# Kernel tuning notes

Measured on AMD Instinct MI355X. Metric: run time of the kernel, lower is better.

The kernel has to match this reference:

```python
import jax, jax.numpy as jnp
import numpy as np

B, S, D, H = 8, 1024, 512, 12
HS = D // H  # 42 (head_size; 12*42 = 504 concat width, as in the original)


def setup_inputs() -> dict:
    key = jax.random.key(0)
    ks = jax.random.split(key, 12)
    sd = 0.02
    return {
        "embedded_patches": jax.random.normal(ks[0], (B, S, D), dtype=jnp.float32),
        # stacked per-head projections (12 independent Linear(D, HS, bias=False))
        "wk": jax.random.normal(ks[1], (H, D, HS), dtype=jnp.float32) * sd,
        "wq": jax.random.normal(ks[2], (H, D, HS), dtype=jnp.float32) * sd,
        "wv": jax.random.normal(ks[3], (H, D, HS), dtype=jnp.float32) * sd,
        "w_proj": jax.random.normal(ks[4], (H * HS, D), dtype=jnp.float32) * sd,  # [504, 512]
        "b_proj": jnp.zeros((D,), dtype=jnp.float32),
        # shared LayerNorm (same params used for both norms, as in the original)
        "gamma": jnp.ones((D,), dtype=jnp.float32),
        "beta": jnp.zeros((D,), dtype=jnp.float32),
        "w1": jax.random.normal(ks[5], (D, 4 * D), dtype=jnp.float32) * sd,
        "b1": jnp.zeros((4 * D,), dtype=jnp.float32),
        "w2": jax.random.normal(ks[6], (4 * D, D), dtype=jnp.float32) * sd,
        "b2": jnp.zeros((D,), dtype=jnp.float32),
    }


def _layernorm(x, gamma, beta, eps=1e-5):
    mu = jnp.mean(x, axis=-1, keepdims=True)
    var = jnp.var(x, axis=-1, keepdims=True)
    return (x - mu) * jax.lax.rsqrt(var + eps) * gamma + beta


def reference(embedded_patches, wk, wq, wv, w_proj, b_proj, gamma, beta, w1, b1, w2, b2):
    x = embedded_patches
    n1 = _layernorm(x, gamma, beta)
    # per-head projections, vectorized over heads: [B,S,D] x [H,D,E] -> [B,H,S,E]
    q = jnp.einsum('bsd,hde->bhse', n1, wq)
    k = jnp.einsum('bsd,hde->bhse', n1, wk)
    v = jnp.einsum('bsd,hde->bhse', n1, wv)
    scale = HS ** -0.5
    wei = jax.nn.softmax(jnp.einsum('bhse,bhte->bhst', q, k) * scale, axis=-1)
    out = jnp.einsum('bhst,bhte->bhse', wei, v)        # [B,H,S,E]
    out = out.transpose(0, 2, 1, 3).reshape(B, S, H * HS)  # concat heads -> [B,S,504]
    attn = out @ w_proj + b_proj                       # [B,S,D]
    # original quirk: takes batch element 0 and broadcasts against residual
    first_added = attn[0] + x                          # [S,D] + [B,S,D] -> [B,S,D]
    n2 = _layernorm(first_added, gamma, beta)
    h = jax.nn.gelu(n2 @ w1 + b1, approximate=False)   # torch nn.GELU default = exact erf
    ff = h @ w2 + b2
    return ff + first_added
```

## Files before the change

### kernel.cpp

```cpp
#include <hip/hip_runtime.h>
#include <hip/hip_bf16.h>
#include <stdint.h>


typedef unsigned short u16;
typedef __attribute__((ext_vector_type(8))) short short8;
typedef __attribute__((ext_vector_type(4))) float f32x4;

__device__ __forceinline__ u16 f2bf(float f) {
  union { float f; unsigned u; } x; x.f = f;
  return (u16)((x.u + 0x7FFFu + ((x.u >> 16) & 1u)) >> 16);
}
__device__ __forceinline__ float bf2f(u16 u) {
  union { unsigned u; float f; } x; x.u = ((unsigned)u) << 16;
  return x.f;
}

__device__ __forceinline__ void gload_lds16(const u16* g, u16* l) {
  __builtin_amdgcn_global_load_lds(
      (__attribute__((address_space(1))) void*)g,
      (__attribute__((address_space(3))) void*)l, 16, 0, 0);
}

__device__ __forceinline__ float wred_sum(float v) {
#pragma unroll
  for (int off = 32; off > 0; off >>= 1) v += __shfl_xor(v, off, 64);
  return v;
}

__device__ __forceinline__ float gelu_fast(float t) {
  const float p = __builtin_fmaf(0.0356774081f, t * t, 0.7978845608f);
  return t / (1.0f + __expf(-2.0f * t * p));
}

#define MFMA16x16(a, b, c) __builtin_amdgcn_mfma_f32_16x16x32_bf16(a, b, c, 0, 0, 0)

enum { EP_BF16 = 0, EP_F32B = 2, EP_GELU = 3, EP_ATOM = 7 };

template <int EP, int TM>
__device__ __forceinline__ void gemm_core(u16* lds, const u16* __restrict__ Ab,
                                          int lda, const u16* __restrict__ Bb,
                                          int ldb, void* __restrict__ Cv,
                                          int ldc, int K,
                                          const float* __restrict__ bias,
                                          int m0, int n0) {
  constexpr int ASZ = TM * 32;
  u16* lA[2] = {lds, lds + ASZ};
  u16* lB[2] = {lds + 2 * ASZ, lds + 2 * ASZ + 4096};

  const int tid = threadIdx.x;
  const int w = tid >> 6;
  const int l = tid & 63;
  const int wr = w >> 1;
  const int wc = w & 1;
  const int NT = K >> 5;

  f32x4 acc[4][4];
#pragma unroll
  for (int i = 0; i < 4; ++i)
#pragma unroll
    for (int j = 0; j < 4; ++j) acc[i][j] = (f32x4){0.f, 0.f, 0.f, 0.f};

  const int sk = (l & 3) * 8;
  const u16* gA = Ab + (long)(m0 + w * 32 + (l >> 2)) * lda + sk;
  const int dOffA = w * 1024;
  const int srowB = (TM == 128) ? (w * 32 + (l >> 2)) : (w * 16 + (l >> 2));
  const u16* gB = Bb + (long)(n0 + srowB) * ldb + sk;
  const int dOffB = (TM == 128) ? w * 1024 : w * 512;

  const int aoff = (wr * 64 + (l & 15)) * 32 + (l >> 4) * 8;
  const int boff = (wc * 64 + (l & 15)) * 32 + (l >> 4) * 8;

  auto stage = [&](int b_, int t_) {
    const int k0 = t_ * 32;
    gload_lds16(gA + k0, lA[b_] + dOffA);
    gload_lds16(gA + k0 + 16 * lda, lA[b_] + dOffA + 512);
    gload_lds16(gB + k0, lB[b_] + dOffB);
    if (TM == 128) gload_lds16(gB + k0 + 16 * ldb, lB[b_] + dOffB + 512);
  };

  stage(0, 0);
  __syncthreads();

  int buf = 0;
  for (int t = 0; t < NT; ++t) {
    short8 af[4], bfv[4];
#pragma unroll
    for (int mi = 0; mi < 4; ++mi)
      af[mi] = *(const short8*)&lA[buf][aoff + mi * 16 * 32];
#pragma unroll
    for (int ni = 0; ni < 4; ++ni)
      bfv[ni] = *(const short8*)&lB[buf][boff + ni * 16 * 32];
    if (t + 1 < NT) stage(buf ^ 1, t + 1);
#pragma unroll
    for (int mi = 0; mi < 4; ++mi)
#pragma unroll
      for (int ni = 0; ni < 4; ++ni)
        acc[mi][ni] = MFMA16x16(af[mi], bfv[ni], acc[mi][ni]);
    __syncthreads();
    buf ^= 1;
  }

  const int rbase = m0 + wr * 64 + (l >> 4) * 4;
  const int cbase = n0 + wc * 64 + (l & 15);
#pragma unroll
  for (int mi = 0; mi < 4; ++mi) {
#pragma unroll
    for (int ni = 0; ni < 4; ++ni) {
#pragma unroll
      for (int j = 0; j < 4; ++j) {
        const int row = rbase + mi * 16 + j;
        const int col = cbase + ni * 16;
        const float v = acc[mi][ni][j];
        if (EP == EP_BF16) {
          ((u16*)Cv)[(long)row * ldc + col] = f2bf(v);
        } else if (EP == EP_F32B) {
          ((float*)Cv)[(long)row * ldc + col] = v + bias[col];
        } else if (EP == EP_GELU) {
          ((u16*)Cv)[(long)row * ldc + col] = f2bf(gelu_fast(v + bias[col]));
        } else {
          atomicAdd(&((float*)Cv)[(long)row * ldc + col], v);
        }
      }
    }
  }
}

template <int EP, int TM>
__launch_bounds__(TM * 2, 2)
__global__ void gemm_k(const u16* __restrict__ A, int lda, long sAz,
                       const u16* __restrict__ Bt, int ldb, long sBz,
                       void* __restrict__ Cv, int ldc, int K,
                       const float* __restrict__ bias) {
  __shared__ u16 lds[2 * TM * 32 + 2 * 128 * 32];
  const int gx = gridDim.x, gy = gridDim.y, gz = gridDim.z;
  const int lin = blockIdx.x + gx * (blockIdx.y + gy * blockIdx.z);
  const int nwg = gx * gy * gz;
  const int wg = (lin & 7) * (nwg >> 3) + (lin >> 3);
  const int by = wg % gy;
  const int rem = wg / gy;
  const int z = rem % gz;
  const int bx = rem / gz;
  const u16* Ab = A + (long)z * sAz;
  const u16* Bb = Bt + (long)z * sBz;
  gemm_core<EP, TM>(lds, Ab, lda, Bb, ldb, Cv, ldc, K, bias, bx * TM,
                    by * 128);
}

__launch_bounds__(256, 4)
__global__ void qkvt_kernel(const u16* __restrict__ n1,
                            const u16* __restrict__ BtQKV,
                            u16* __restrict__ qkvc,
                            const u16* __restrict__ wvT,
                            u16* __restrict__ vt) {
  __shared__ u16 lds[4 * 128 * 32];
  const int lin = blockIdx.x;
  const int wg = (lin & 7) * 24 + (lin >> 3);
  if (wg < 96) {
    gemm_core<EP_BF16, 128>(lds, n1, 512, BtQKV, 512, qkvc, 1536, 512,
                            nullptr, (wg & 7) * 128, (wg >> 3) * 128);
  } else {
    const int v = wg - 96;
    gemm_core<EP_BF16, 128>(lds, wvT, 512, n1, 512, vt, 1024, 512, nullptr,
                            (v % 12) * 128, (v / 12) * 128);
  }
}

__device__ __forceinline__ short8 frag_read(const u16* base, int row, int ks,
                                            int l) {
  const int g = (ks * 4 + (l >> 4)) ^ (l & 7);
  return *(const short8*)&base[row * 64 + g * 8];
}

__launch_bounds__(256, 2)
__global__ void flash_attn(const u16* __restrict__ qkvc,
                           const u16* __restrict__ vt,
                           u16* __restrict__ cat) {
  __shared__ u16 lQ[64 * 64];
  __shared__ u16 lK[2][64 * 64];
  __shared__ u16 lV[2][64 * 64];
  __shared__ u16 lP[4][16 * 64];
  const int h = blockIdx.x;
  const int q0 = blockIdx.y * 64;
  const int tid = threadIdx.x;
  const int w = tid >> 6;
  const int l = tid & 63;
  const int sg = ((l & 7) ^ (l >> 3)) * 8;
  const int sr = w * 8 + (l >> 3);

#define FA_STAGE(t_, b_)                                                    \
  do {                                                                      \
    const int kv_ = (t_) * 64;                                              \
    gload_lds16(qkvc + (long)(kv_ + sr) * 1536 + 768 + h * 64 + sg,         \
                lK[b_] + w * 8 * 64);                                       \
    gload_lds16(qkvc + (long)(kv_ + 32 + sr) * 1536 + 768 + h * 64 + sg,    \
                lK[b_] + (32 + w * 8) * 64);                                \
    gload_lds16(vt + (long)(h * 128 + sr) * 1024 + kv_ + sg,                \
                lV[b_] + w * 8 * 64);                                       \
    gload_lds16(vt + (long)(h * 128 + 32 + sr) * 1024 + kv_ + sg,           \
                lV[b_] + (32 + w * 8) * 64);                                \
  } while (0)

  gload_lds16(qkvc + (long)(q0 + sr) * 1536 + h * 64 + sg, lQ + w * 8 * 64);
  gload_lds16(qkvc + (long)(q0 + 32 + sr) * 1536 + h * 64 + sg,
              lQ + (32 + w * 8) * 64);
  FA_STAGE(0, 0);
  __syncthreads();

  const short8 qf0 = frag_read(lQ, w * 16 + (l & 15), 0, l);
  const short8 qf1 = frag_read(lQ, w * 16 + (l & 15), 1, l);

  f32x4 accO[4];
  float m_run[4], l_run[4];
#pragma unroll
  for (int i = 0; i < 4; ++i) {
    accO[i] = (f32x4){0.f, 0.f, 0.f, 0.f};
    m_run[i] = -3.0e38f;
    l_run[i] = 0.f;
  }

  int buf = 0;
  for (int t = 0; t < 16; ++t) {
    if (t + 1 < 16) FA_STAGE(t + 1, buf ^ 1);
    f32x4 s[4];
#pragma unroll
    for (int ni = 0; ni < 4; ++ni) {
      const short8 kf0 = frag_read(lK[buf], ni * 16 + (l & 15), 0, l);
      const short8 kf1 = frag_read(lK[buf], ni * 16 + (l & 15), 1, l);
      s[ni] = MFMA16x16(qf0, kf0, ((f32x4){0.f, 0.f, 0.f, 0.f}));
      s[ni] = MFMA16x16(qf1, kf1, s[ni]);
    }
#pragma unroll
    for (int j = 0; j < 4; ++j) {
      float mx = fmaxf(fmaxf(s[0][j], s[1][j]), fmaxf(s[2][j], s[3][j]));
      mx = fmaxf(mx, __shfl_xor(mx, 1));
      mx = fmaxf(mx, __shfl_xor(mx, 2));
      mx = fmaxf(mx, __shfl_xor(mx, 4));
      mx = fmaxf(mx, __shfl_xor(mx, 8));
      const float mn = fmaxf(m_run[j], mx);
      const float corr = __expf(m_run[j] - mn);
      m_run[j] = mn;
      float ps = 0.f;
#pragma unroll
      for (int ni = 0; ni < 4; ++ni) {
        const float p = __expf(s[ni][j] - mn);
        s[ni][j] = p;
        ps += p;
      }
      ps += __shfl_xor(ps, 1);
      ps += __shfl_xor(ps, 2);
      ps += __shfl_xor(ps, 4);
      ps += __shfl_xor(ps, 8);
      l_run[j] = l_run[j] * corr + ps;
#pragma unroll
      for (int ne = 0; ne < 4; ++ne) accO[ne][j] *= corr;
    }
#pragma unroll
    for (int ni = 0; ni < 4; ++ni) {
#pragma unroll
      for (int j = 0; j < 4; ++j) {
        const int row = (l >> 4) * 4 + j;
        const int col = ni * 16 + (l & 15);
        const int boff = row * 128 + (((col >> 3) ^ (row & 7)) << 4) +
                         (col & 7) * 2;
        *(u16*)((char*)lP[w] + boff) = f2bf(s[ni][j]);
      }
    }
    asm volatile("s_waitcnt lgkmcnt(0)" ::: "memory");
    __builtin_amdgcn_sched_barrier(0);
    const short8 pf0 = frag_read(lP[w], (l & 15), 0, l);
    const short8 pf1 = frag_read(lP[w], (l & 15), 1, l);
#pragma unroll
    for (int ne = 0; ne < 4; ++ne) {
      const short8 vf0 = frag_read(lV[buf], ne * 16 + (l & 15), 0, l);
      const short8 vf1 = frag_read(lV[buf], ne * 16 + (l & 15), 1, l);
      accO[ne] = MFMA16x16(pf0, vf0, accO[ne]);
      accO[ne] = MFMA16x16(pf1, vf1, accO[ne]);
    }
    __syncthreads();
    buf ^= 1;
  }
#undef FA_STAGE

#pragma unroll
  for (int j = 0; j < 4; ++j) {
    const float inv = 1.0f / l_run[j];
    const int row = q0 + w * 16 + (l >> 4) * 4 + j;
#pragma unroll
    for (int ne = 0; ne < 4; ++ne) {
      const int e = ne * 16 + (l & 15);
      if (e < 42)
        cat[(long)row * 512 + h * 42 + e] = f2bf(accO[ne][j] * inv);
    }
  }
}

__device__ __forceinline__ void transpose_body(const float* __restrict__ in,
                                               u16* __restrict__ out, int N,
                                               int Kin, int Kpad, int blk,
                                               int gx, int t, float* smem) {
  const int n0 = (blk % gx) * 64;
  const int k0 = (blk / gx) * 64;
  const int tc = t & 63;
  const int tr = t >> 6;
#pragma unroll
  for (int r = 0; r < 16; ++r) {
    const int kr = tr * 16 + r;
    const int kg = k0 + kr;
    smem[kr * 65 + tc] = (kg < Kin) ? in[(long)kg * N + n0 + tc] : 0.f;
  }
  __syncthreads();
  const int nr0 = t >> 4;
  const int kc = (t & 15) * 4;
#pragma unroll
  for (int p = 0; p < 4; ++p) {
    const int nr = nr0 + p * 16;
    ushort4 v;
    v.x = f2bf(smem[(kc + 0) * 65 + nr]);
    v.y = f2bf(smem[(kc + 1) * 65 + nr]);
    v.z = f2bf(smem[(kc + 2) * 65 + nr]);
    v.w = f2bf(smem[(kc + 3) * 65 + nr]);
    *(ushort4*)&out[(long)(n0 + nr) * Kpad + k0 + kc] = v;
  }
}

__global__ void prep_fused(const float* __restrict__ wq,
                           const float* __restrict__ wk,
                           const float* __restrict__ wv,
                           const float* __restrict__ w_proj,
                           const float* __restrict__ w1,
                           const float* __restrict__ w2,
                           const float* __restrict__ x,
                           const float* __restrict__ gamma,
                           const float* __restrict__ beta,
                           u16* __restrict__ BtQKV, u16* __restrict__ wvT,
                           u16* __restrict__ BtP, u16* __restrict__ Bt1,
                           u16* __restrict__ Bt2, u16* __restrict__ cat,
                           u16* __restrict__ n1, float scale) {
  __shared__ float smem[64 * 65];
  const int blk = blockIdx.x;
  const int t = threadIdx.x;
  if (blk < 3072) {
    const int i = blk * 256 + t;
    const int n = i >> 9, d = i & 511;
    const int pq = n / 768;
    const int h = (n % 768) >> 6;
    const int e = n & 63;
    float v = 0.f;
    if (e < 42) {
      v = (pq ? wk : wq)[((long)h * 512 + d) * 42 + e];
      if (!pq) v *= scale;
    }
    BtQKV[i] = f2bf(v);
  } else if (blk < 6144) {
    const int i = (blk - 3072) * 256 + t;
    const int r = i >> 9, d = i & 511;
    const int h = r >> 7, e = r & 127;
    wvT[i] = f2bf(e < 42 ? wv[((long)h * 512 + d) * 42 + e] : 0.f);
  } else if (blk < 6208) {
    transpose_body(w_proj, BtP, 512, 504, 512, blk - 6144, 8, t, smem);
  } else if (blk < 6464) {
    transpose_body(w1, Bt1, 2048, 512, 512, blk - 6208, 32, t, smem);
  } else if (blk < 6720) {
    transpose_body(w2, Bt2, 512, 2048, 2048, blk - 6464, 8, t, smem);
  } else if (blk < 8768) {
    cat[(blk - 6720) * 256 + t] = 0;
  } else {
    const int s = blk - 8768;
    const float* row = x + (long)s * 512;
    const float v0 = row[t];
    const float v1 = row[t + 256];
    float sum = wred_sum(v0 + v1);
    float sq = wred_sum(v0 * v0 + v1 * v1);
    if ((t & 63) == 0) { smem[t >> 6] = sum; smem[8 + (t >> 6)] = sq; }
    __syncthreads();
    sum = smem[0] + smem[1] + smem[2] + smem[3];
    sq = smem[8] + smem[9] + smem[10] + smem[11];
    const float mu = sum * (1.0f / 512.0f);
    const float rstd = rsqrtf(sq * (1.0f / 512.0f) - mu * mu + 1e-5f);
    n1[(long)s * 512 + t] = f2bf((v0 - mu) * rstd * gamma[t] + beta[t]);
    n1[(long)s * 512 + t + 256] =
        f2bf((v1 - mu) * rstd * gamma[t + 256] + beta[t + 256]);
  }
}

__global__ void ln2_kernel(const float* __restrict__ x,
                           const float* __restrict__ aproj,
                           const float* __restrict__ gamma,
                           const float* __restrict__ beta,
                           const float* __restrict__ b2,
                           u16* __restrict__ n2, float* __restrict__ outp) {
  __shared__ float red[16];
  const int r = blockIdx.x;
  const int t = threadIdx.x;
  const int s = r & 1023;
  const float* xr = x + (long)r * 512;
  const float* ar = aproj + (long)s * 512;
  const float v0 = xr[t] + ar[t];
  const float v1 = xr[t + 256] + ar[t + 256];
  outp[(long)r * 512 + t] = v0 + b2[t];
  outp[(long)r * 512 + t + 256] = v1 + b2[t + 256];
  float sum = wred_sum(v0 + v1);
  float sq = wred_sum(v0 * v0 + v1 * v1);
  if ((t & 63) == 0) { red[t >> 6] = sum; red[8 + (t >> 6)] = sq; }
  __syncthreads();
  sum = red[0] + red[1] + red[2] + red[3];
  sq = red[8] + red[9] + red[10] + red[11];
  const float mu = sum * (1.0f / 512.0f);
  const float rstd = rsqrtf(sq * (1.0f / 512.0f) - mu * mu + 1e-5f);
  n2[(long)r * 512 + t] = f2bf((v0 - mu) * rstd * gamma[t] + beta[t]);
  n2[(long)r * 512 + t + 256] =
      f2bf((v1 - mu) * rstd * gamma[t + 256] + beta[t + 256]);
}

extern "C" void kernel_launch(void* const* d_in, const int* in_sizes, int n_in,
                              void* d_out, int out_size, void* d_ws,
                              size_t ws_size, hipStream_t stream) {
  const float* x = (const float*)d_in[0];
  const float* wk = (const float*)d_in[1];
  const float* wq = (const float*)d_in[2];
  const float* wv = (const float*)d_in[3];
  const float* w_proj = (const float*)d_in[4];
  const float* b_proj = (const float*)d_in[5];
  const float* gamma = (const float*)d_in[6];
  const float* beta = (const float*)d_in[7];
  const float* w1 = (const float*)d_in[8];
  const float* b1 = (const float*)d_in[9];
  const float* w2 = (const float*)d_in[10];
  const float* b2 = (const float*)d_in[11];

  char* base = (char*)d_ws;
  size_t off = 0;
  auto alloc = [&](size_t bytes) -> void* {
    void* p = base + off;
    off += (bytes + 255) & ~(size_t)255;
    return p;
  };
  u16* n1 = (u16*)alloc(1024L * 512 * 2);
  u16* qkvc = (u16*)alloc(1024L * 1536 * 2);
  u16* wvT = (u16*)alloc(1536L * 512 * 2);
  u16* vt = (u16*)alloc(1536L * 1024 * 2);
  u16* cat = (u16*)alloc(1024L * 512 * 2);
  float* aproj = (float*)alloc(1024L * 512 * 4);
  u16* n2 = (u16*)alloc(8192L * 512 * 2);
  u16* hbuf = (u16*)alloc(8192L * 2048 * 2);
  u16* BtQKV = (u16*)alloc(1536L * 512 * 2);
  u16* BtP = (u16*)alloc(512L * 512 * 2);
  u16* Bt1 = (u16*)alloc(2048L * 512 * 2);
  u16* Bt2 = (u16*)alloc(512L * 2048 * 2);
  (void)ws_size; (void)in_sizes; (void)n_in; (void)out_size;

  const float scale = 0.15430334996209191f;

  prep_fused<<<9792, 256, 0, stream>>>(wq, wk, wv, w_proj, w1, w2, x, gamma,
                                       beta, BtQKV, wvT, BtP, Bt1, Bt2, cat,
                                       n1, scale);
  qkvt_kernel<<<192, 256, 0, stream>>>(n1, BtQKV, qkvc, wvT, vt);
  flash_attn<<<dim3(12, 16), 256, 0, stream>>>(qkvc, vt, cat);
  gemm_k<EP_F32B, 128><<<dim3(8, 4, 1), 256, 0, stream>>>(
      cat, 512, 0, BtP, 512, 0, aproj, 512, 512, b_proj);
  ln2_kernel<<<8192, 256, 0, stream>>>(x, aproj, gamma, beta, b2, n2,
                                       (float*)d_out);
  gemm_k<EP_GELU, 256><<<dim3(32, 16, 1), 512, 0, stream>>>(
      n2, 512, 0, Bt1, 512, 0, hbuf, 2048, 512, b1);
  gemm_k<EP_ATOM, 256><<<dim3(32, 4, 2), 512, 0, stream>>>(
      hbuf, 2048, 1024, Bt2, 2048, 1024, d_out, 512, 1024, nullptr);
}
```

Before: 173.0 us.

## Use 128x128 GEMM tiles everywhere and restructure weight-prep transposes through LDS

Drops the 256-row tile variant so the FFN GEMMs run as 256-thread 128x128 workgroups (twice as many blocks), with launch bounds raised to 5 waves per SIMD for more occupancy. The QKV and V weight repacking now stages 64-row slabs in shared memory so both reads and writes are coalesced, using far fewer blocks. The cat buffer zeroing now clears only the 8 padding columns, since attention writes the rest. This trades per-tile reuse of B loads in the FFN GEMMs for better occupancy and load balance, and cuts prep-kernel memory traffic.

New measurement: 377.3 us. +118.1%, slower.

```diff
diff --git a/kernel.cpp b/kernel.cpp
--- a/kernel.cpp
+++ b/kernel.cpp
@@ -37,16 +37,15 @@
 
 enum { EP_BF16 = 0, EP_F32B = 2, EP_GELU = 3, EP_ATOM = 7 };
 
-template <int EP, int TM>
+template <int EP>
 __device__ __forceinline__ void gemm_core(u16* lds, const u16* __restrict__ Ab,
                                           int lda, const u16* __restrict__ Bb,
                                           int ldb, void* __restrict__ Cv,
                                           int ldc, int K,
                                           const float* __restrict__ bias,
                                           int m0, int n0) {
-  constexpr int ASZ = TM * 32;
-  u16* lA[2] = {lds, lds + ASZ};
-  u16* lB[2] = {lds + 2 * ASZ, lds + 2 * ASZ + 4096};
+  u16* lA[2] = {lds, lds + 4096};
+  u16* lB[2] = {lds + 8192, lds + 12288};
 
   const int tid = threadIdx.x;
   const int w = tid >> 6;
@@ -61,22 +60,21 @@
 #pragma unroll
     for (int j = 0; j < 4; ++j) acc[i][j] = (f32x4){0.f, 0.f, 0.f, 0.f};
 
+  const int srow = w * 32 + (l >> 2);
   const int sk = (l & 3) * 8;
-  const u16* gA = Ab + (long)(m0 + w * 32 + (l >> 2)) * lda + sk;
-  const int dOffA = w * 1024;
-  const int srowB = (TM == 128) ? (w * 32 + (l >> 2)) : (w * 16 + (l >> 2));
-  const u16* gB = Bb + (long)(n0 + srowB) * ldb + sk;
-  const int dOffB = (TM == 128) ? w * 1024 : w * 512;
+  const u16* gA = Ab + (long)(m0 + srow) * lda + sk;
+  const u16* gB = Bb + (long)(n0 + srow) * ldb + sk;
+  const int dOff = w * 1024;
 
   const int aoff = (wr * 64 + (l & 15)) * 32 + (l >> 4) * 8;
   const int boff = (wc * 64 + (l & 15)) * 32 + (l >> 4) * 8;
 
   auto stage = [&](int b_, int t_) {
     const int k0 = t_ * 32;
-    gload_lds16(gA + k0, lA[b_] + dOffA);
-    gload_lds16(gA + k0 + 16 * lda, lA[b_] + dOffA + 512);
-    gload_lds16(gB + k0, lB[b_] + dOffB);
-    if (TM == 128) gload_lds16(gB + k0 + 16 * ldb, lB[b_] + dOffB + 512);
+    gload_lds16(gA + k0, lA[b_] + dOff);
+    gload_lds16(gA + k0 + 16 * lda, lA[b_] + dOff + 512);
+    gload_lds16(gB + k0, lB[b_] + dOff);
+    gload_lds16(gB + k0 + 16 * ldb, lB[b_] + dOff + 512);
   };
 
   stage(0, 0);
@@ -126,13 +124,13 @@
   }
 }
 
-template <int EP, int TM>
-__launch_bounds__(TM * 2, 2)
+template <int EP>
+__launch_bounds__(256, 5)
 __global__ void gemm_k(const u16* __restrict__ A, int lda, long sAz,
                        const u16* __restrict__ Bt, int ldb, long sBz,
                        void* __restrict__ Cv, int ldc, int K,
                        const float* __restrict__ bias) {
-  __shared__ u16 lds[2 * TM * 32 + 2 * 128 * 32];
+  __shared__ u16 lds[4 * 128 * 32];
   const int gx = gridDim.x, gy = gridDim.y, gz = gridDim.z;
   const int lin = blockIdx.x + gx * (blockIdx.y + gy * blockIdx.z);
   const int nwg = gx * gy * gz;
@@ -143,11 +141,10 @@
   const int bx = rem / gz;
   const u16* Ab = A + (long)z * sAz;
   const u16* Bb = Bt + (long)z * sBz;
-  gemm_core<EP, TM>(lds, Ab, lda, Bb, ldb, Cv, ldc, K, bias, bx * TM,
-                    by * 128);
-}
-
-__launch_bounds__(256, 4)
+  gemm_core<EP>(lds, Ab, lda, Bb, ldb, Cv, ldc, K, bias, bx * 128, by * 128);
+}
+
+__launch_bounds__(256, 5)
 __global__ void qkvt_kernel(const u16* __restrict__ n1,
                             const u16* __restrict__ BtQKV,
                             u16* __restrict__ qkvc,
@@ -157,12 +154,12 @@
   const int lin = blockIdx.x;
   const int wg = (lin & 7) * 24 + (lin >> 3);
   if (wg < 96) {
-    gemm_core<EP_BF16, 128>(lds, n1, 512, BtQKV, 512, qkvc, 1536, 512,
-                            nullptr, (wg & 7) * 128, (wg >> 3) * 128);
+    gemm_core<EP_BF16>(lds, n1, 512, BtQKV, 512, qkvc, 1536, 512, nullptr,
+                       (wg & 7) * 128, (wg >> 3) * 128);
   } else {
     const int v = wg - 96;
-    gemm_core<EP_BF16, 128>(lds, wvT, 512, n1, 512, vt, 1024, 512, nullptr,
-                            (v % 12) * 128, (v / 12) * 128);
+    gemm_core<EP_BF16>(lds, wvT, 512, n1, 512, vt, 1024, 512, nullptr,
+                       (v % 12) * 128, (v / 12) * 128);
   }
 }
 
@@ -340,33 +337,47 @@
   __shared__ float smem[64 * 65];
   const int blk = blockIdx.x;
   const int t = threadIdx.x;
-  if (blk < 3072) {
-    const int i = blk * 256 + t;
-    const int n = i >> 9, d = i & 511;
-    const int pq = n / 768;
-    const int h = (n % 768) >> 6;
-    const int e = n & 63;
-    float v = 0.f;
-    if (e < 42) {
-      v = (pq ? wk : wq)[((long)h * 512 + d) * 42 + e];
-      if (!pq) v *= scale;
-    }
-    BtQKV[i] = f2bf(v);
-  } else if (blk < 6144) {
-    const int i = (blk - 3072) * 256 + t;
-    const int r = i >> 9, d = i & 511;
-    const int h = r >> 7, e = r & 127;
-    wvT[i] = f2bf(e < 42 ? wv[((long)h * 512 + d) * 42 + e] : 0.f);
-  } else if (blk < 6208) {
-    transpose_body(w_proj, BtP, 512, 504, 512, blk - 6144, 8, t, smem);
-  } else if (blk < 6464) {
-    transpose_body(w1, Bt1, 2048, 512, 512, blk - 6208, 32, t, smem);
-  } else if (blk < 6720) {
-    transpose_body(w2, Bt2, 512, 2048, 2048, blk - 6464, 8, t, smem);
-  } else if (blk < 8768) {
-    cat[(blk - 6720) * 256 + t] = 0;
+  if (blk < 192) {
+    const int pq = blk / 96;
+    const int rem = blk % 96;
+    const int h = rem >> 3;
+    const int d0 = (rem & 7) * 64;
+    const float* src = (pq ? wk : wq) + ((long)h * 512 + d0) * 42;
+    for (int i = t; i < 2688; i += 256) smem[(i / 42) * 43 + (i % 42)] = src[i];
+    __syncthreads();
+    const float sc = pq ? 1.0f : scale;
+    const int d = t & 63;
+#pragma unroll
+    for (int p = 0; p < 16; ++p) {
+      const int e = (t >> 6) + p * 4;
+      const float v = (e < 42) ? smem[d * 43 + e] * sc : 0.f;
+      BtQKV[((long)(pq * 768 + h * 64 + e)) * 512 + d0 + d] = f2bf(v);
+    }
+  } else if (blk < 288) {
+    const int b = blk - 192;
+    const int h = b >> 3;
+    const int d0 = (b & 7) * 64;
+    const float* src = wv + ((long)h * 512 + d0) * 42;
+    for (int i = t; i < 2688; i += 256) smem[(i / 42) * 43 + (i % 42)] = src[i];
+    __syncthreads();
+    const int d = t & 63;
+#pragma unroll
+    for (int p = 0; p < 32; ++p) {
+      const int e = (t >> 6) + p * 4;
+      const float v = (e < 42) ? smem[d * 43 + e] : 0.f;
+      wvT[((long)(h * 128 + e)) * 512 + d0 + d] = f2bf(v);
+    }
+  } else if (blk < 352) {
+    transpose_body(w_proj, BtP, 512, 504, 512, blk - 288, 8, t, smem);
+  } else if (blk < 608) {
+    transpose_body(w1, Bt1, 2048, 512, 512, blk - 352, 32, t, smem);
+  } else if (blk < 864) {
+    transpose_body(w2, Bt2, 512, 2048, 2048, blk - 608, 8, t, smem);
+  } else if (blk < 896) {
+    const int i = (blk - 864) * 256 + t;
+    cat[(long)(i >> 3) * 512 + 504 + (i & 7)] = 0;
   } else {
-    const int s = blk - 8768;
+    const int s = blk - 896;
     const float* row = x + (long)s * 512;
     const float v0 = row[t];
     const float v1 = row[t + 256];
@@ -452,17 +463,17 @@
 
   const float scale = 0.15430334996209191f;
 
-  prep_fused<<<9792, 256, 0, stream>>>(wq, wk, wv, w_proj, w1, w2, x, gamma,
+  prep_fused<<<1920, 256, 0, stream>>>(wq, wk, wv, w_proj, w1, w2, x, gamma,
                                        beta, BtQKV, wvT, BtP, Bt1, Bt2, cat,
                                        n1, scale);
   qkvt_kernel<<<192, 256, 0, stream>>>(n1, BtQKV, qkvc, wvT, vt);
   flash_attn<<<dim3(12, 16), 256, 0, stream>>>(qkvc, vt, cat);
-  gemm_k<EP_F32B, 128><<<dim3(8, 4, 1), 256, 0, stream>>>(
+  gemm_k<EP_F32B><<<dim3(8, 4, 1), 256, 0, stream>>>(
       cat, 512, 0, BtP, 512, 0, aproj, 512, 512, b_proj);
   ln2_kernel<<<8192, 256, 0, stream>>>(x, aproj, gamma, beta, b2, n2,
                                        (float*)d_out);
-  gemm_k<EP_GELU, 256><<<dim3(32, 16, 1), 512, 0, stream>>>(
+  gemm_k<EP_GELU><<<dim3(64, 16, 1), 256, 0, stream>>>(
       n2, 512, 0, Bt1, 512, 0, hbuf, 2048, 512, b1);
-  gemm_k<EP_ATOM, 256><<<dim3(32, 4, 2), 512, 0, stream>>>(
+  gemm_k<EP_ATOM><<<dim3(64, 4, 2), 256, 0, stream>>>(
       hbuf, 2048, 1024, Bt2, 2048, 1024, d_out, 512, 1024, nullptr);
 }
```
